# Optimization experiments

Measured on AMD Instinct MI355X. Metric: run time of the kernel, lower is better.

Reference implementation:

```python
import jax, jax.numpy as jnp
import numpy as np

MARGIN_SCALE = 0.2
SPATIAL_ALPHA = 0.6
CHANNEL_ALPHA = 0.5
LANG_ALPHA = 0.4
EPS = 1e-06


def _xywh_to_xyxy(boxes):
    xc, yc, w, h = jnp.split(boxes, 4, axis=-1)
    return jnp.concatenate([xc - w / 2.0, yc - h / 2.0, xc + w / 2.0, yc + h / 2.0], axis=-1)


def _clamp_boxes(boxes):
    x1, y1, x2, y2 = [jnp.clip(b[..., 0], 0.0, 1.0) for b in jnp.split(boxes, 4, axis=-1)]
    x_low, x_high = jnp.minimum(x1, x2), jnp.maximum(x1, x2)
    y_low, y_high = jnp.minimum(y1, y2), jnp.maximum(y1, y2)
    w = jnp.maximum(x_high - x_low, EPS)
    h = jnp.maximum(y_high - y_low, EPS)
    cx = (x_high + x_low) * 0.5
    cy = (y_high + y_low) * 0.5
    return jnp.stack([
        jnp.clip(cx - w * 0.5, 0.0, 1.0),
        jnp.clip(cy - h * 0.5, 0.0, 1.0),
        jnp.clip(cx + w * 0.5, 0.0, 1.0),
        jnp.clip(cy + h * 0.5, 0.0, 1.0),
    ], axis=-1)


def _box_to_mask(boxes_xyxy, H, W, margin, dtype):
    # fully vectorized replacement of the per-sample Python loop
    ys = jnp.linspace(0.0, 1.0, H)  # [H]
    xs = jnp.linspace(0.0, 1.0, W)  # [W]
    x1, y1, x2, y2 = [boxes_xyxy[:, i] for i in range(4)]
    mx1 = jnp.clip(x1 - margin, 0.0, 1.0)[:, None, None]
    my1 = jnp.clip(y1 - margin, 0.0, 1.0)[:, None, None]
    mx2 = jnp.clip(x2 + margin, 0.0, 1.0)[:, None, None]
    my2 = jnp.clip(y2 + margin, 0.0, 1.0)[:, None, None]
    xg = xs[None, None, :]  # [1,1,W]
    yg = ys[None, :, None]  # [1,H,1]
    mask = (xg >= mx1) & (xg <= mx2) & (yg >= my1) & (yg <= my2)  # [B,H,W]
    return mask.astype(dtype)[:, None, :, :]  # [B,1,H,W]


def _conv2d(x, w, b, pad):
    out = jax.lax.conv_general_dilated(
        x, w, window_strides=(1, 1), padding=((pad, pad), (pad, pad)),
        dimension_numbers=('NCHW', 'OIHW', 'NCHW'))
    return out + b[None, :, None, None]


def setup_inputs() -> dict:
    key = jax.random.key(0)
    ks = jax.random.split(key, 9)
    B, C, H, W = 32, 256, 64, 64
    s = lambda fan_in: 1.0 / np.sqrt(fan_in)
    return {
        'feat': jax.random.normal(ks[0], (B, C, H, W), jnp.float32),
        'lang_vec': jax.random.normal(ks[1], (B, 256), jnp.float32),
        'pointer_xywh': jax.random.uniform(ks[2], (B, 4), jnp.float32),
        'conv1_w': jax.random.normal(ks[3], (16, 1, 3, 3), jnp.float32) * s(9),
        'conv1_b': jnp.zeros((16,), jnp.float32),
        'conv2_w': jax.random.normal(ks[4], (1, 16, 1, 1), jnp.float32) * s(16),
        'conv2_b': jnp.zeros((1,), jnp.float32),
        'cg_w1': jax.random.normal(ks[5], (256, 512), jnp.float32) * s(512),
        'cg_b1': jnp.zeros((256,), jnp.float32),
        'cg_w2': jax.random.normal(ks[6], (256, 256), jnp.float32) * s(256),
        'cg_b2': jnp.zeros((256,), jnp.float32),
        'lf_w1': jax.random.normal(ks[7], (256, 512), jnp.float32) * s(512),
        'lf_b1': jnp.zeros((256,), jnp.float32),
        'lf_w2': jax.random.normal(ks[8], (256, 256), jnp.float32) * s(256),
        'lf_b2': jnp.zeros((256,), jnp.float32),
    }


def reference(feat, lang_vec, pointer_xywh, conv1_w, conv1_b, conv2_w, conv2_b,
              cg_w1, cg_b1, cg_w2, cg_b2, lf_w1, lf_b1, lf_w2, lf_b2):
    B, C, H, W = feat.shape
    boxes_xyxy = _clamp_boxes(_xywh_to_xyxy(pointer_xywh))
    w = jnp.maximum(boxes_xyxy[:, 2] - boxes_xyxy[:, 0], 1e-4)
    h = jnp.maximum(boxes_xyxy[:, 3] - boxes_xyxy[:, 1], 1e-4)
    diag = jnp.sqrt(w * w + h * h)
    margin = jnp.clip(diag * MARGIN_SCALE, 0.02, 0.2)
    mask = _box_to_mask(boxes_xyxy, H, W, margin, feat.dtype)  # [B,1,H,W]

    # spatial gate: conv3x3 -> relu -> conv1x1 -> sigmoid
    hidden = jax.nn.relu(_conv2d(mask, conv1_w, conv1_b, pad=1))
    refined_mask = jax.nn.sigmoid(_conv2d(hidden, conv2_w, conv2_b, pad=0))  # [B,1,H,W]

    mask_area = jnp.maximum(refined_mask.sum(axis=(2, 3)), 1.0)  # [B,1]
    pointer_feat = (feat * refined_mask).sum(axis=(2, 3)) / mask_area  # [B,C]

    fusion = jnp.concatenate([pointer_feat, lang_vec], axis=1)  # [B, C+256]
    ch_gate = jax.nn.sigmoid(jax.nn.relu(fusion @ cg_w1.T + cg_b1) @ cg_w2.T + cg_b2)
    ch_gate = ch_gate.reshape(B, C, 1, 1)
    lang_delta = jnp.tanh(jax.nn.relu(fusion @ lf_w1.T + lf_b1) @ lf_w2.T + lf_b2)

    guided_feat = feat * (1.0 + SPATIAL_ALPHA * refined_mask) * (1.0 + CHANNEL_ALPHA * ch_gate)
    guided_lang = lang_vec + LANG_ALPHA * lang_delta
    return (guided_feat, guided_lang, boxes_xyxy, refined_mask, pointer_feat)
```

## Files before the change

### kernel.cpp

```cpp
#include <hip/hip_runtime.h>
#include <hip/hip_cooperative_groups.h>
#include <math.h>

#define B_  32
#define C_  256
#define H_  64
#define W_  64
#define HW  (H_*W_)
#define HW4 (HW/4)
#define MRPB 8
#define RPB 4

namespace cg = cooperative_groups;

typedef float f32x4 __attribute__((ext_vector_type(4)));

__device__ __forceinline__ float clamp01(float v) {
    return fminf(fmaxf(v, 0.0f), 1.0f);
}

struct BoxParams {
    float bx1, by1, bx2, by2, mx1, my1, mx2, my2;
};

__device__ __forceinline__ BoxParams box_math(const float* __restrict__ xywh, int b) {
    const float xc = xywh[b * 4 + 0];
    const float yc = xywh[b * 4 + 1];
    const float bw = xywh[b * 4 + 2];
    const float bh = xywh[b * 4 + 3];

    float x1 = clamp01(xc - bw * 0.5f);
    float y1 = clamp01(yc - bh * 0.5f);
    float x2 = clamp01(xc + bw * 0.5f);
    float y2 = clamp01(yc + bh * 0.5f);
    float xl = fminf(x1, x2), xh = fmaxf(x1, x2);
    float yl = fminf(y1, y2), yh = fmaxf(y1, y2);
    float w_ = fmaxf(xh - xl, 1e-6f);
    float h_ = fmaxf(yh - yl, 1e-6f);
    float cx = (xh + xl) * 0.5f, cy = (yh + yl) * 0.5f;
    BoxParams p;
    p.bx1 = clamp01(cx - w_ * 0.5f);
    p.by1 = clamp01(cy - h_ * 0.5f);
    p.bx2 = clamp01(cx + w_ * 0.5f);
    p.by2 = clamp01(cy + h_ * 0.5f);
    float ww = fmaxf(p.bx2 - p.bx1, 1e-4f);
    float hh = fmaxf(p.by2 - p.by1, 1e-4f);
    float diag = sqrtf(ww * ww + hh * hh);
    float margin = fminf(fmaxf(diag * 0.2f, 0.02f), 0.2f);
    p.mx1 = clamp01(p.bx1 - margin);
    p.my1 = clamp01(p.by1 - margin);
    p.mx2 = clamp01(p.bx2 + margin);
    p.my2 = clamp01(p.by2 + margin);
    return p;
}

__device__ __forceinline__ void build_tables(
    int t, const BoxParams& p, float b2v,
    const float* sw1, const float* sb1, const float* sw2,
    int* xpat, int* ypat, float* tbl)
{
    if (t < 64) {
        const int x = t;
        int pp = 0;
        #pragma unroll
        for (int k = 0; k < 3; ++k) {
            const int xx = x + k - 1;
            float gx = (float)((double)xx / 63.0);
            bool in = (xx >= 0) && (xx < W_) && (gx >= p.mx1) && (gx <= p.mx2);
            pp |= (in ? 1 : 0) << k;
        }
        xpat[x] = pp;
    } else if (t < 128) {
        const int y = t - 64;
        int pp = 0;
        #pragma unroll
        for (int k = 0; k < 3; ++k) {
            const int yy = y + k - 1;
            float gy = (float)((double)yy / 63.0);
            bool in = (yy >= 0) && (yy < H_) && (gy >= p.my1) && (gy <= p.my2);
            pp |= (in ? 1 : 0) << k;
        }
        ypat[y] = pp;
    } else if (t < 192) {
        const int e = t - 128;
        const int xp = e & 7, yp = e >> 3;
        float mv[9];
        #pragma unroll
        for (int ky = 0; ky < 3; ++ky)
            #pragma unroll
            for (int kx = 0; kx < 3; ++kx)
                mv[ky * 3 + kx] = (((yp >> ky) & 1) && ((xp >> kx) & 1)) ? 1.0f : 0.0f;
        float z = b2v;
        #pragma unroll
        for (int oc = 0; oc < 16; ++oc) {
            float hsum = sb1[oc];
            #pragma unroll
            for (int k = 0; k < 9; ++k) hsum = fmaf(mv[k], sw1[oc * 9 + k], hsum);
            z = fmaf(fmaxf(hsum, 0.0f), sw2[oc], z);
        }
        tbl[e] = 1.0f / (1.0f + expf(-z));
    }
}

__global__ __launch_bounds__(256, 4) void kern_mega(
    const float* __restrict__ feat, const float* __restrict__ lang,
    const float* __restrict__ xywh,
    const float* __restrict__ conv1_w, const float* __restrict__ conv1_b,
    const float* __restrict__ conv2_w, const float* __restrict__ conv2_b,
    const float* __restrict__ cg_w1, const float* __restrict__ cg_b1,
    const float* __restrict__ cg_w2, const float* __restrict__ cg_b2,
    const float* __restrict__ lf_w1, const float* __restrict__ lf_b1,
    const float* __restrict__ lf_w2, const float* __restrict__ lf_b2,
    float* __restrict__ out_gf, float* __restrict__ out_gl,
    float* __restrict__ out_boxes, float* __restrict__ out_rm,
    float* __restrict__ out_pf, float* __restrict__ ws_cg)
{
    cg::grid_group grid = cg::this_grid();

    const int blk = blockIdx.x;
    const int b = blk >> 5;
    const int g = blk & 31;
    const int c0 = g * MRPB;
    const int t = threadIdx.x;

    __shared__ f32x4 rm4_lds[HW4];
    __shared__ __align__(16) char scratch[3072];

    float* sw1   = (float*)(scratch);
    float* sb1   = (float*)(scratch + 576);
    float* sw2   = (float*)(scratch + 640);
    float* tbl   = (float*)(scratch + 704);
    int*   xpat  = (int*)  (scratch + 960);
    int*   ypat  = (int*)  (scratch + 1216);
    float* sreda = (float*)(scratch + 1472);
    float* sredp = (float*)(scratch + 1536);
    float* fus   = (float*)(scratch);
    float* hid   = (float*)(scratch + 2048);

    float* rm_lds = (float*)rm4_lds;

    if (t < 144)                 sw1[t]       = conv1_w[t];
    else if (t < 160)            sb1[t - 144] = conv1_b[t - 144];
    else if (t < 176)            sw2[t - 160] = conv2_w[t - 160];
    const float b2v = conv2_b[0];

    const BoxParams bp = box_math(xywh, b);
    if (t == 0 && g == 0) {
        out_boxes[b * 4 + 0] = bp.bx1;
        out_boxes[b * 4 + 1] = bp.by1;
        out_boxes[b * 4 + 2] = bp.bx2;
        out_boxes[b * 4 + 3] = bp.by2;
    }
    __syncthreads();

    build_tables(t, bp, b2v, sw1, sb1, sw2, xpat, ypat, tbl);
    __syncthreads();

    float asum = 0.0f;
    for (int p = t; p < HW; p += 256) {
        const int y = p >> 6;
        const int x = p & 63;
        float rm = tbl[ypat[y] * 8 + xpat[x]];
        rm_lds[p] = rm;
        asum += rm;
    }
    #pragma unroll
    for (int off = 32; off > 0; off >>= 1) asum += __shfl_down(asum, off, 64);
    const int lane = t & 63, wid = t >> 6;
    if (lane == 0) sreda[wid] = asum;
    __syncthreads();
    const float inv = 1.0f / fmaxf(sreda[0] + sreda[1] + sreda[2] + sreda[3], 1.0f);

    if (g == 0) {
        f32x4* orm = (f32x4*)(out_rm + (size_t)b * HW);
        for (int i = t; i < HW4; i += 256) orm[i] = rm4_lds[i];
    }

    const size_t row0 = ((size_t)b * C_ + c0) * HW;
    const f32x4* fr = (const f32x4*)(feat + row0);
    {
        float s[MRPB];
        #pragma unroll
        for (int j = 0; j < MRPB; ++j) s[j] = 0.0f;
        for (int i = t; i < HW4; i += 256) {
            f32x4 r = rm4_lds[i];
            #pragma unroll
            for (int j = 0; j < MRPB; ++j) {
                f32x4 f = fr[i + j * HW4];
                s[j] = fmaf(f.x, r.x, fmaf(f.y, r.y, fmaf(f.z, r.z, fmaf(f.w, r.w, s[j]))));
            }
        }
        #pragma unroll
        for (int j = 0; j < MRPB; ++j) {
            #pragma unroll
            for (int off = 32; off > 0; off >>= 1) s[j] += __shfl_down(s[j], off, 64);
        }
        if (lane == 0) {
            #pragma unroll
            for (int j = 0; j < MRPB; ++j) sredp[wid * MRPB + j] = s[j];
        }
        __syncthreads();
        if (t < MRPB) {
            float tot = sredp[0 * MRPB + t] + sredp[1 * MRPB + t] +
                        sredp[2 * MRPB + t] + sredp[3 * MRPB + t];
            out_pf[b * C_ + c0 + t] = tot * inv;
        }
    }

    grid.sync();

    if (blk < 64) {
        const int bb = blk >> 1;
        const int which = blk & 1;

        fus[t]       = out_pf[bb * 256 + t];
        fus[256 + t] = lang[bb * 256 + t];

        const float* w1 = which ? lf_w1 : cg_w1;
        const float* b1 = which ? lf_b1 : cg_b1;
        const float* w2 = which ? lf_w2 : cg_w2;
        const float* b2 = which ? lf_b2 : cg_b2;
        __syncthreads();

        const f32x4* wv = (const f32x4*)(w1 + (size_t)t * 512);
        const f32x4* fv = (const f32x4*)fus;
        float s = 0.0f;
        #pragma unroll 4
        for (int k = 0; k < 128; ++k) {
            f32x4 f = fv[k], w = wv[k];
            s = fmaf(f.x, w.x, fmaf(f.y, w.y, fmaf(f.z, w.z, fmaf(f.w, w.w, s))));
        }
        hid[t] = fmaxf(s + b1[t], 0.0f);
        __syncthreads();

        const f32x4* w2v = (const f32x4*)(w2 + (size_t)t * 256);
        const f32x4* hv = (const f32x4*)hid;
        float s2 = 0.0f;
        #pragma unroll 4
        for (int k = 0; k < 64; ++k) {
            f32x4 h = hv[k], w = w2v[k];
            s2 = fmaf(h.x, w.x, fmaf(h.y, w.y, fmaf(h.z, w.z, fmaf(h.w, w.w, s2))));
        }
        s2 += b2[t];
        if (which == 0) {
            ws_cg[bb * 256 + t] = 1.0f + 0.5f / (1.0f + expf(-s2));
        } else {
            out_gl[bb * 256 + t] = fus[256 + t] + 0.4f * tanhf(s2);
        }
    }

    grid.sync();

    float gr[MRPB];
    #pragma unroll
    for (int j = 0; j < MRPB; ++j) gr[j] = ws_cg[b * C_ + c0 + j];

    f32x4* orow = (f32x4*)(out_gf + row0);
    for (int i = t; i < HW4; i += 256) {
        f32x4 r = rm4_lds[i];
        f32x4 m;
        m.x = 1.0f + 0.6f * r.x;
        m.y = 1.0f + 0.6f * r.y;
        m.z = 1.0f + 0.6f * r.z;
        m.w = 1.0f + 0.6f * r.w;
        #pragma unroll
        for (int j = 0; j < MRPB; ++j) {
            f32x4 f = fr[i + j * HW4];
            f32x4 o;
            o.x = f.x * m.x * gr[j];
            o.y = f.y * m.y * gr[j];
            o.z = f.z * m.z * gr[j];
            o.w = f.w * m.w * gr[j];
            __builtin_nontemporal_store(o, &orow[i + j * HW4]);
        }
    }
}

__global__ __launch_bounds__(256) void kern_pf(
    const float* __restrict__ feat, const float* __restrict__ xywh,
    const float* __restrict__ conv1_w, const float* __restrict__ conv1_b,
    const float* __restrict__ conv2_w, const float* __restrict__ conv2_b,
    float* __restrict__ out_boxes, float* __restrict__ out_rm,
    float* __restrict__ out_pf)
{
    const int blk = blockIdx.x;
    const int b = blk >> 6;
    const int g = blk & 63;
    const int c0 = g * RPB;
    const int t = threadIdx.x;

    __shared__ float sw1[16 * 9];
    __shared__ float sb1[16];
    __shared__ float sw2[16];
    __shared__ float tbl[64];
    __shared__ int   xpat[64];
    __shared__ int   ypat[64];
    __shared__ f32x4 rm4_lds[HW4];
    __shared__ float sreda[4];
    __shared__ f32x4 sredv[4];

    float* rm_lds = (float*)rm4_lds;

    if (t < 144)                 sw1[t]       = conv1_w[t];
    else if (t < 160)            sb1[t - 144] = conv1_b[t - 144];
    else if (t < 176)            sw2[t - 160] = conv2_w[t - 160];
    const float b2v = conv2_b[0];

    const BoxParams bp = box_math(xywh, b);
    if (t == 0 && g == 0) {
        out_boxes[b * 4 + 0] = bp.bx1;
        out_boxes[b * 4 + 1] = bp.by1;
        out_boxes[b * 4 + 2] = bp.bx2;
        out_boxes[b * 4 + 3] = bp.by2;
    }
    __syncthreads();

    build_tables(t, bp, b2v, sw1, sb1, sw2, xpat, ypat, tbl);
    __syncthreads();

    float asum = 0.0f;
    for (int p = t; p < HW; p += 256) {
        const int y = p >> 6;
        const int x = p & 63;
        float rm = tbl[ypat[y] * 8 + xpat[x]];
        rm_lds[p] = rm;
        asum += rm;
    }
    #pragma unroll
    for (int off = 32; off > 0; off >>= 1) asum += __shfl_down(asum, off, 64);
    const int lane = t & 63, wid = t >> 6;
    if (lane == 0) sreda[wid] = asum;
    __syncthreads();
    const float inv = 1.0f / fmaxf(sreda[0] + sreda[1] + sreda[2] + sreda[3], 1.0f);

    if (g == 0) {
        f32x4* orm = (f32x4*)(out_rm + (size_t)b * HW);
        for (int i = t; i < HW4; i += 256) orm[i] = rm4_lds[i];
    }

    const f32x4* fr = (const f32x4*)(feat + ((size_t)b * C_ + c0) * HW);
    float s0 = 0.f, s1 = 0.f, s2 = 0.f, s3 = 0.f;
    #pragma unroll 2
    for (int i = t; i < HW4; i += 256) {
        f32x4 r = rm4_lds[i];
        f32x4 f0 = fr[i];
        f32x4 f1 = fr[i + HW4];
        f32x4 f2 = fr[i + 2 * HW4];
        f32x4 f3 = fr[i + 3 * HW4];
        s0 = fmaf(f0.x, r.x, fmaf(f0.y, r.y, fmaf(f0.z, r.z, fmaf(f0.w, r.w, s0))));
        s1 = fmaf(f1.x, r.x, fmaf(f1.y, r.y, fmaf(f1.z, r.z, fmaf(f1.w, r.w, s1))));
        s2 = fmaf(f2.x, r.x, fmaf(f2.y, r.y, fmaf(f2.z, r.z, fmaf(f2.w, r.w, s2))));
        s3 = fmaf(f3.x, r.x, fmaf(f3.y, r.y, fmaf(f3.z, r.z, fmaf(f3.w, r.w, s3))));
    }
    #pragma unroll
    for (int off = 32; off > 0; off >>= 1) {
        s0 += __shfl_down(s0, off, 64);
        s1 += __shfl_down(s1, off, 64);
        s2 += __shfl_down(s2, off, 64);
        s3 += __shfl_down(s3, off, 64);
    }
    if (lane == 0) { f32x4 v; v.x = s0; v.y = s1; v.z = s2; v.w = s3; sredv[wid] = v; }
    __syncthreads();
    if (t == 0) {
        f32x4 t0 = sredv[0], t1 = sredv[1], t2 = sredv[2], t3 = sredv[3];
        out_pf[b * C_ + c0 + 0] = (t0.x + t1.x + t2.x + t3.x) * inv;
        out_pf[b * C_ + c0 + 1] = (t0.y + t1.y + t2.y + t3.y) * inv;
        out_pf[b * C_ + c0 + 2] = (t0.z + t1.z + t2.z + t3.z) * inv;
        out_pf[b * C_ + c0 + 3] = (t0.w + t1.w + t2.w + t3.w) * inv;
    }
}

__global__ __launch_bounds__(256) void kern_mlp(
    const float* __restrict__ pf, const float* __restrict__ lang,
    const float* __restrict__ cg_w1, const float* __restrict__ cg_b1,
    const float* __restrict__ cg_w2, const float* __restrict__ cg_b2,
    const float* __restrict__ lf_w1, const float* __restrict__ lf_b1,
    const float* __restrict__ lf_w2, const float* __restrict__ lf_b2,
    float* __restrict__ ws_cg, float* __restrict__ out_gl)
{
    const int b = blockIdx.x >> 1;
    const int which = blockIdx.x & 1;
    const int t = threadIdx.x;
    __shared__ float fus[512];
    __shared__ float hid[256];

    fus[t]       = pf[b * 256 + t];
    fus[256 + t] = lang[b * 256 + t];

    const float* w1 = which ? lf_w1 : cg_w1;
    const float* b1 = which ? lf_b1 : cg_b1;
    const float* w2 = which ? lf_w2 : cg_w2;
    const float* b2 = which ? lf_b2 : cg_b2;
    __syncthreads();

    const f32x4* wv = (const f32x4*)(w1 + (size_t)t * 512);
    const f32x4* fv = (const f32x4*)fus;
    float s = 0.0f;
    #pragma unroll 4
    for (int k = 0; k < 128; ++k) {
        f32x4 f = fv[k], w = wv[k];
        s = fmaf(f.x, w.x, fmaf(f.y, w.y, fmaf(f.z, w.z, fmaf(f.w, w.w, s))));
    }
    hid[t] = fmaxf(s + b1[t], 0.0f);
    __syncthreads();

    const f32x4* w2v = (const f32x4*)(w2 + (size_t)t * 256);
    const f32x4* hv = (const f32x4*)hid;
    float s2 = 0.0f;
    #pragma unroll 4
    for (int k = 0; k < 64; ++k) {
        f32x4 h = hv[k], w = w2v[k];
        s2 = fmaf(h.x, w.x, fmaf(h.y, w.y, fmaf(h.z, w.z, fmaf(h.w, w.w, s2))));
    }
    s2 += b2[t];
    if (which == 0) {
        ws_cg[b * 256 + t] = 1.0f + 0.5f / (1.0f + expf(-s2));
    } else {
        out_gl[b * 256 + t] = fus[256 + t] + 0.4f * tanhf(s2);
    }
}

__global__ __launch_bounds__(256) void kern_guided(
    const float* __restrict__ feat, const float* __restrict__ rm,
    const float* __restrict__ ws_cg, float* __restrict__ out_gf)
{
    const int blk = blockIdx.x;
    const int b = blk >> 6;
    const int c0 = (blk & 63) * RPB;
    const float g0 = ws_cg[b * C_ + c0 + 0];
    const float g1 = ws_cg[b * C_ + c0 + 1];
    const float g2 = ws_cg[b * C_ + c0 + 2];
    const float g3 = ws_cg[b * C_ + c0 + 3];

    const size_t row0 = ((size_t)b * C_ + c0) * HW;
    const f32x4* fr = (const f32x4*)(feat + row0);
    f32x4* orow = (f32x4*)(out_gf + row0);
    const f32x4* r4 = (const f32x4*)(rm + (size_t)b * HW);

    #pragma unroll 2
    for (int i = threadIdx.x; i < HW4; i += 256) {
        f32x4 r = r4[i];
        f32x4 m;
        m.x = 1.0f + 0.6f * r.x;
        m.y = 1.0f + 0.6f * r.y;
        m.z = 1.0f + 0.6f * r.z;
        m.w = 1.0f + 0.6f * r.w;
        f32x4 f0 = fr[i];
        f32x4 f1 = fr[i + HW4];
        f32x4 f2 = fr[i + 2 * HW4];
        f32x4 f3 = fr[i + 3 * HW4];
        f32x4 o0, o1, o2, o3;
        o0.x = f0.x * m.x * g0; o0.y = f0.y * m.y * g0;
        o0.z = f0.z * m.z * g0; o0.w = f0.w * m.w * g0;
        o1.x = f1.x * m.x * g1; o1.y = f1.y * m.y * g1;
        o1.z = f1.z * m.z * g1; o1.w = f1.w * m.w * g1;
        o2.x = f2.x * m.x * g2; o2.y = f2.y * m.y * g2;
        o2.z = f2.z * m.z * g2; o2.w = f2.w * m.w * g2;
        o3.x = f3.x * m.x * g3; o3.y = f3.y * m.y * g3;
        o3.z = f3.z * m.z * g3; o3.w = f3.w * m.w * g3;
        __builtin_nontemporal_store(o0, &orow[i]);
        __builtin_nontemporal_store(o1, &orow[i + HW4]);
        __builtin_nontemporal_store(o2, &orow[i + 2 * HW4]);
        __builtin_nontemporal_store(o3, &orow[i + 3 * HW4]);
    }
}

extern "C" void kernel_launch(void* const* d_in, const int* in_sizes, int n_in,
                              void* d_out, int out_size, void* d_ws, size_t ws_size,
                              hipStream_t stream) {
    const float* feat     = (const float*)d_in[0];
    const float* lang     = (const float*)d_in[1];
    const float* xywh     = (const float*)d_in[2];
    const float* conv1_w  = (const float*)d_in[3];
    const float* conv1_b  = (const float*)d_in[4];
    const float* conv2_w  = (const float*)d_in[5];
    const float* conv2_b  = (const float*)d_in[6];
    const float* cg_w1    = (const float*)d_in[7];
    const float* cg_b1    = (const float*)d_in[8];
    const float* cg_w2    = (const float*)d_in[9];
    const float* cg_b2    = (const float*)d_in[10];
    const float* lf_w1    = (const float*)d_in[11];
    const float* lf_b1    = (const float*)d_in[12];
    const float* lf_w2    = (const float*)d_in[13];
    const float* lf_b2    = (const float*)d_in[14];

    float* out = (float*)d_out;
    const size_t N_GF = (size_t)B_ * C_ * HW;
    float* out_gf    = out;
    float* out_gl    = out_gf + N_GF;
    float* out_boxes = out_gl + (size_t)B_ * C_;
    float* out_rm    = out_boxes + B_ * 4;
    float* out_pf    = out_rm + (size_t)B_ * HW;

    float* ws_cg = (float*)d_ws;

    (void)ws_size; (void)in_sizes; (void)n_in; (void)out_size;

    const int MEGA_GRID = B_ * C_ / MRPB;
    int nb = 0;
    hipError_t oe = hipOccupancyMaxActiveBlocksPerMultiprocessor(&nb, kern_mega, 256, 0);
    const bool coop_ok = (oe == hipSuccess) && (nb * 256 >= MEGA_GRID);

    if (coop_ok) {
        void* args[] = {
            (void*)&feat, (void*)&lang, (void*)&xywh,
            (void*)&conv1_w, (void*)&conv1_b, (void*)&conv2_w, (void*)&conv2_b,
            (void*)&cg_w1, (void*)&cg_b1, (void*)&cg_w2, (void*)&cg_b2,
            (void*)&lf_w1, (void*)&lf_b1, (void*)&lf_w2, (void*)&lf_b2,
            (void*)&out_gf, (void*)&out_gl, (void*)&out_boxes, (void*)&out_rm,
            (void*)&out_pf, (void*)&ws_cg
        };
        hipLaunchCooperativeKernel((const void*)kern_mega,
                                   dim3(MEGA_GRID), dim3(256),
                                   args, 0, stream);
    } else {
        kern_pf<<<B_ * C_ / RPB, 256, 0, stream>>>(feat, xywh,
                                                   conv1_w, conv1_b, conv2_w, conv2_b,
                                                   out_boxes, out_rm, out_pf);
        kern_mlp<<<B_ * 2, 256, 0, stream>>>(out_pf, lang,
                                             cg_w1, cg_b1, cg_w2, cg_b2,
                                             lf_w1, lf_b1, lf_w2, lf_b2,
                                             ws_cg, out_gl);
        kern_guided<<<B_ * C_ / RPB, 256, 0, stream>>>(feat, out_rm, ws_cg, out_gf);
    }
}
```

Baseline: 94.29 us.

## Replace grid-wide syncs with per-batch last-block counter and flag spin-wait

Removes the two cooperative grid.sync barriers and replaces them with a per-batch atomic counter: the last block to finish its pointer-feature slice runs both MLPs for that batch and then sets a flag, while the other blocks of that batch spin on the flag. The kernel is templated on rows per block, and the host picks 4 rows per block (2048 blocks) when occupancy allows, otherwise 8. The aim is to let each batch proceed on its own instead of waiting on the whole grid, and to give more blocks to hide latency. It adds a memset of the counters on every call and depends on all blocks being co-resident, since blocks spin-wait on each other.

```diff
diff --git a/kernel.cpp b/kernel.cpp
--- a/kernel.cpp
+++ b/kernel.cpp
@@ -8,10 +8,7 @@
 #define W_  64
 #define HW  (H_*W_)
 #define HW4 (HW/4)
-#define MRPB 8
-#define RPB 4
-
-namespace cg = cooperative_groups;
+#define FRPB 4
 
 typedef float f32x4 __attribute__((ext_vector_type(4)));
 
@@ -102,6 +99,7 @@
     }
 }
 
+template<int RPB>
 __global__ __launch_bounds__(256, 4) void kern_mega(
     const float* __restrict__ feat, const float* __restrict__ lang,
     const float* __restrict__ xywh,
@@ -113,18 +111,19 @@
     const float* __restrict__ lf_w2, const float* __restrict__ lf_b2,
     float* __restrict__ out_gf, float* __restrict__ out_gl,
     float* __restrict__ out_boxes, float* __restrict__ out_rm,
-    float* __restrict__ out_pf, float* __restrict__ ws_cg)
+    float* __restrict__ out_pf, float* __restrict__ ws_cg,
+    int* __restrict__ cnt, int* __restrict__ flag)
 {
-    cg::grid_group grid = cg::this_grid();
-
+    constexpr int GPB = C_ / RPB;
     const int blk = blockIdx.x;
-    const int b = blk >> 5;
-    const int g = blk & 31;
-    const int c0 = g * MRPB;
+    const int b = blk / GPB;
+    const int g = blk % GPB;
+    const int c0 = g * RPB;
     const int t = threadIdx.x;
 
     __shared__ f32x4 rm4_lds[HW4];
     __shared__ __align__(16) char scratch[3072];
+    __shared__ int is_last;
 
     float* sw1   = (float*)(scratch);
     float* sb1   = (float*)(scratch + 576);
@@ -179,81 +178,114 @@
     const size_t row0 = ((size_t)b * C_ + c0) * HW;
     const f32x4* fr = (const f32x4*)(feat + row0);
     {
-        float s[MRPB];
-        #pragma unroll
-        for (int j = 0; j < MRPB; ++j) s[j] = 0.0f;
+        float s[RPB];
+        #pragma unroll
+        for (int j = 0; j < RPB; ++j) s[j] = 0.0f;
         for (int i = t; i < HW4; i += 256) {
             f32x4 r = rm4_lds[i];
             #pragma unroll
-            for (int j = 0; j < MRPB; ++j) {
+            for (int j = 0; j < RPB; ++j) {
                 f32x4 f = fr[i + j * HW4];
                 s[j] = fmaf(f.x, r.x, fmaf(f.y, r.y, fmaf(f.z, r.z, fmaf(f.w, r.w, s[j]))));
             }
         }
         #pragma unroll
-        for (int j = 0; j < MRPB; ++j) {
+        for (int j = 0; j < RPB; ++j) {
             #pragma unroll
             for (int off = 32; off > 0; off >>= 1) s[j] += __shfl_down(s[j], off, 64);
         }
         if (lane == 0) {
             #pragma unroll
-            for (int j = 0; j < MRPB; ++j) sredp[wid * MRPB + j] = s[j];
+            for (int j = 0; j < RPB; ++j) sredp[wid * RPB + j] = s[j];
         }
         __syncthreads();
-        if (t < MRPB) {
-            float tot = sredp[0 * MRPB + t] + sredp[1 * MRPB + t] +
-                        sredp[2 * MRPB + t] + sredp[3 * MRPB + t];
+        if (t < RPB) {
+            float tot = sredp[0 * RPB + t] + sredp[1 * RPB + t] +
+                        sredp[2 * RPB + t] + sredp[3 * RPB + t];
             out_pf[b * C_ + c0 + t] = tot * inv;
         }
     }
-
-    grid.sync();
-
-    if (blk < 64) {
-        const int bb = blk >> 1;
-        const int which = blk & 1;
-
-        fus[t]       = out_pf[bb * 256 + t];
-        fus[256 + t] = lang[bb * 256 + t];
-
-        const float* w1 = which ? lf_w1 : cg_w1;
-        const float* b1 = which ? lf_b1 : cg_b1;
-        const float* w2 = which ? lf_w2 : cg_w2;
-        const float* b2 = which ? lf_b2 : cg_b2;
+    __syncthreads();
+
+    if (t == 0) {
+        __threadfence();
+        int old = __hip_atomic_fetch_add(&cnt[b], 1, __ATOMIC_ACQ_REL,
+                                         __HIP_MEMORY_SCOPE_AGENT);
+        is_last = (old == GPB - 1) ? 1 : 0;
+    }
+    __syncthreads();
+
+    if (is_last) {
+        __threadfence();
+        fus[t]       = out_pf[b * 256 + t];
+        fus[256 + t] = lang[b * 256 + t];
         __syncthreads();
 
-        const f32x4* wv = (const f32x4*)(w1 + (size_t)t * 512);
         const f32x4* fv = (const f32x4*)fus;
-        float s = 0.0f;
-        #pragma unroll 4
-        for (int k = 0; k < 128; ++k) {
-            f32x4 f = fv[k], w = wv[k];
-            s = fmaf(f.x, w.x, fmaf(f.y, w.y, fmaf(f.z, w.z, fmaf(f.w, w.w, s))));
-        }
-        hid[t] = fmaxf(s + b1[t], 0.0f);
+        {
+            const f32x4* wv = (const f32x4*)(cg_w1 + (size_t)t * 512);
+            float sa = 0.0f, sb = 0.0f;
+            #pragma unroll 4
+            for (int k = 0; k < 128; k += 2) {
+                f32x4 f0 = fv[k],   w0 = wv[k];
+                f32x4 f1 = fv[k+1], w1 = wv[k+1];
+                sa = fmaf(f0.x, w0.x, fmaf(f0.y, w0.y, fmaf(f0.z, w0.z, fmaf(f0.w, w0.w, sa))));
+                sb = fmaf(f1.x, w1.x, fmaf(f1.y, w1.y, fmaf(f1.z, w1.z, fmaf(f1.w, w1.w, sb))));
+            }
+            hid[t] = fmaxf(sa + sb + cg_b1[t], 0.0f);
+            __syncthreads();
+            const f32x4* w2v = (const f32x4*)(cg_w2 + (size_t)t * 256);
+            const f32x4* hv = (const f32x4*)hid;
+            float s2 = 0.0f;
+            #pragma unroll 4
+            for (int k = 0; k < 64; ++k) {
+                f32x4 h = hv[k], w = w2v[k];
+                s2 = fmaf(h.x, w.x, fmaf(h.y, w.y, fmaf(h.z, w.z, fmaf(h.w, w.w, s2))));
+            }
+            s2 += cg_b2[t];
+            ws_cg[b * 256 + t] = 1.0f + 0.5f / (1.0f + expf(-s2));
+        }
         __syncthreads();
-
-        const f32x4* w2v = (const f32x4*)(w2 + (size_t)t * 256);
-        const f32x4* hv = (const f32x4*)hid;
-        float s2 = 0.0f;
-        #pragma unroll 4
-        for (int k = 0; k < 64; ++k) {
-            f32x4 h = hv[k], w = w2v[k];
-            s2 = fmaf(h.x, w.x, fmaf(h.y, w.y, fmaf(h.z, w.z, fmaf(h.w, w.w, s2))));
-        }
-        s2 += b2[t];
-        if (which == 0) {
-            ws_cg[bb * 256 + t] = 1.0f + 0.5f / (1.0f + expf(-s2));
-        } else {
-            out_gl[bb * 256 + t] = fus[256 + t] + 0.4f * tanhf(s2);
-        }
-    }
-
-    grid.sync();
-
-    float gr[MRPB];
+        {
+            const f32x4* wv = (const f32x4*)(lf_w1 + (size_t)t * 512);
+            float sa = 0.0f, sb = 0.0f;
+            #pragma unroll 4
+            for (int k = 0; k < 128; k += 2) {
+                f32x4 f0 = fv[k],   w0 = wv[k];
+                f32x4 f1 = fv[k+1], w1 = wv[k+1];
+                sa = fmaf(f0.x, w0.x, fmaf(f0.y, w0.y, fmaf(f0.z, w0.z, fmaf(f0.w, w0.w, sa))));
+                sb = fmaf(f1.x, w1.x, fmaf(f1.y, w1.y, fmaf(f1.z, w1.z, fmaf(f1.w, w1.w, sb))));
+            }
+            hid[t] = fmaxf(sa + sb + lf_b1[t], 0.0f);
+            __syncthreads();
+            const f32x4* w2v = (const f32x4*)(lf_w2 + (size_t)t * 256);
+            const f32x4* hv = (const f32x4*)hid;
+            float s2 = 0.0f;
+            #pragma unroll 4
+            for (int k = 0; k < 64; ++k) {
+                f32x4 h = hv[k], w = w2v[k];
+                s2 = fmaf(h.x, w.x, fmaf(h.y, w.y, fmaf(h.z, w.z, fmaf(h.w, w.w, s2))));
+            }
+            s2 += lf_b2[t];
+            out_gl[b * 256 + t] = fus[256 + t] + 0.4f * tanhf(s2);
+        }
+        __syncthreads();
+        __threadfence();
+        if (t == 0)
+            __hip_atomic_store(&flag[b], 1, __ATOMIC_RELEASE, __HIP_MEMORY_SCOPE_AGENT);
+    }
+
+    if (t == 0) {
+        while (__hip_atomic_load(&flag[b], __ATOMIC_ACQUIRE,
+                                 __HIP_MEMORY_SCOPE_AGENT) == 0) {
+            __builtin_amdgcn_s_sleep(8);
+        }
+    }
+    __syncthreads();
+
+    float gr[RPB];
     #pragma unroll
-    for (int j = 0; j < MRPB; ++j) gr[j] = ws_cg[b * C_ + c0 + j];
+    for (int j = 0; j < RPB; ++j) gr[j] = ws_cg[b * C_ + c0 + j];
 
     f32x4* orow = (f32x4*)(out_gf + row0);
     for (int i = t; i < HW4; i += 256) {
@@ -264,7 +296,7 @@
         m.z = 1.0f + 0.6f * r.z;
         m.w = 1.0f + 0.6f * r.w;
         #pragma unroll
-        for (int j = 0; j < MRPB; ++j) {
+        for (int j = 0; j < RPB; ++j) {
             f32x4 f = fr[i + j * HW4];
             f32x4 o;
             o.x = f.x * m.x * gr[j];
@@ -286,7 +318,7 @@
     const int blk = blockIdx.x;
     const int b = blk >> 6;
     const int g = blk & 63;
-    const int c0 = g * RPB;
+    const int c0 = g * FRPB;
     const int t = threadIdx.x;
 
     __shared__ float sw1[16 * 9];
@@ -426,7 +458,7 @@
 {
     const int blk = blockIdx.x;
     const int b = blk >> 6;
-    const int c0 = (blk & 63) * RPB;
+    const int c0 = (blk & 63) * FRPB;
     const float g0 = ws_cg[b * C_ + c0 + 0];
     const float g1 = ws_cg[b * C_ + c0 + 1];
     const float g2 = ws_cg[b * C_ + c0 + 2];
@@ -492,35 +524,44 @@
     float* out_rm    = out_boxes + B_ * 4;
     float* out_pf    = out_rm + (size_t)B_ * HW;
 
-    float* ws_cg = (float*)d_ws;
+    int*   cnt   = (int*)d_ws;
+    int*   flag  = cnt + 32;
+    float* ws_cg = (float*)(flag + 32);
 
     (void)ws_size; (void)in_sizes; (void)n_in; (void)out_size;
 
-    const int MEGA_GRID = B_ * C_ / MRPB;
-    int nb = 0;
-    hipError_t oe = hipOccupancyMaxActiveBlocksPerMultiprocessor(&nb, kern_mega, 256, 0);
-    const bool coop_ok = (oe == hipSuccess) && (nb * 256 >= MEGA_GRID);
-
-    if (coop_ok) {
+    int nb4 = 0, nb8 = 0;
+    hipOccupancyMaxActiveBlocksPerMultiprocessor(&nb4, kern_mega<4>, 256, 0);
+    hipOccupancyMaxActiveBlocksPerMultiprocessor(&nb8, kern_mega<8>, 256, 0);
+
+    const bool use4 = (nb4 * 256 >= 2048);
+    const bool use8 = (nb8 * 256 >= 1024);
+
+    if (use4 || use8) {
+        hipMemsetAsync(d_ws, 0, 256, stream);
         void* args[] = {
             (void*)&feat, (void*)&lang, (void*)&xywh,
             (void*)&conv1_w, (void*)&conv1_b, (void*)&conv2_w, (void*)&conv2_b,
             (void*)&cg_w1, (void*)&cg_b1, (void*)&cg_w2, (void*)&cg_b2,
             (void*)&lf_w1, (void*)&lf_b1, (void*)&lf_w2, (void*)&lf_b2,
             (void*)&out_gf, (void*)&out_gl, (void*)&out_boxes, (void*)&out_rm,
-            (void*)&out_pf, (void*)&ws_cg
+            (void*)&out_pf, (void*)&ws_cg, (void*)&cnt, (void*)&flag
         };
-        hipLaunchCooperativeKernel((const void*)kern_mega,
-                                   dim3(MEGA_GRID), dim3(256),
-                                   args, 0, stream);
+        if (use4) {
+            hipLaunchCooperativeKernel((const void*)kern_mega<4>,
+                                       dim3(2048), dim3(256), args, 0, stream);
+        } else {
+            hipLaunchCooperativeKernel((const void*)kern_mega<8>,
+                                       dim3(1024), dim3(256), args, 0, stream);
+        }
     } else {
-        kern_pf<<<B_ * C_ / RPB, 256, 0, stream>>>(feat, xywh,
-                                                   conv1_w, conv1_b, conv2_w, conv2_b,
-                                                   out_boxes, out_rm, out_pf);
+        kern_pf<<<B_ * C_ / FRPB, 256, 0, stream>>>(feat, xywh,
+                                                    conv1_w, conv1_b, conv2_w, conv2_b,
+                                                    out_boxes, out_rm, out_pf);
         kern_mlp<<<B_ * 2, 256, 0, stream>>>(out_pf, lang,
                                              cg_w1, cg_b1, cg_w2, cg_b2,
                                              lf_w1, lf_b1, lf_w2, lf_b2,
                                              ws_cg, out_gl);
-        kern_guided<<<B_ * C_ / RPB, 256, 0, stream>>>(feat, out_rm, ws_cg, out_gf);
-    }
-}
+        kern_guided<<<B_ * C_ / FRPB, 256, 0, stream>>>(feat, out_rm, ws_cg, out_gf);
+    }
+}
```

Result: no change. 94.47 us (+0.2%).
